# Kernel tuning notes

Hardware: AMD Instinct MI355X
Metric: run time of the kernel (lower is better)

The kernel has to match this reference:

```python
import jax, jax.numpy as jnp
import numpy as np

B, N_ATOMS, D_ATOM = 64, 256, 256
T_ANGLES = 2048
D_HID, D_OUT = 512, 256
BN_EPS = 1e-5


def setup_inputs() -> dict:
    key = jax.random.key(0)
    ks = jax.random.split(key, 8)
    z = jax.random.normal(ks[0], (B, N_ATOMS, D_ATOM), dtype=jnp.float32)
    # all entries valid (>=0) so the nonzero-selected row set is all B*T rows
    angel_atom_table = jax.random.randint(ks[1], (B, T_ANGLES, 3), 0, N_ATOMS, dtype=jnp.int64)
    W1 = jax.random.normal(ks[2], (D_ATOM, D_HID), dtype=jnp.float32) * (1.0 / np.sqrt(D_ATOM))
    b1 = jax.random.normal(ks[3], (D_HID,), dtype=jnp.float32) * 0.01
    gamma = jnp.ones((D_HID,), dtype=jnp.float32)
    beta = jnp.zeros((D_HID,), dtype=jnp.float32)
    W2 = jax.random.normal(ks[4], (D_HID, D_OUT), dtype=jnp.float32) * (1.0 / np.sqrt(D_HID))
    b2 = jax.random.normal(ks[5], (D_OUT,), dtype=jnp.float32) * 0.01
    return {"z": z, "angel_atom_table": angel_atom_table, "W1": W1, "b1": b1,
            "gamma": gamma, "beta": beta, "W2": W2, "b2": b2}


def reference(z, angel_atom_table, W1, b1, gamma, beta, W2, b2):
    Bb, Tt, _ = angel_atom_table.shape
    bi = jnp.arange(Bb)[:, None]                       # [B,1] broadcast batch index
    # gather 3 atom embeddings per angle and sum -> [B,T,d_atom]
    x = (z[bi, angel_atom_table[:, :, 0]]
         + z[bi, angel_atom_table[:, :, 1]]
         + z[bi, angel_atom_table[:, :, 2]])
    x = x.reshape(Bb * Tt, -1)                         # flattened valid rows (all valid)
    h = x @ W1 + b1                                    # Linear(d_atom, d_hid)
    mean = jnp.mean(h, axis=0)                         # BatchNorm1d (batch stats)
    var = jnp.var(h, axis=0)
    h = (h - mean) * jax.lax.rsqrt(var + BN_EPS) * gamma + beta
    h = jax.nn.relu(h)                                 # dropout inactive (eval)
    out = h @ W2 + b2                                  # Linear(d_hid, d_output)
    return out
```

## Files before the change

kernel.cpp:

```cpp
#include <hip/hip_runtime.h>

static constexpr int Bn  = 64;
static constexpr int T   = 2048;
static constexpr int NA  = 256;
static constexpr int DA  = 256;
static constexpr int DH  = 512;
static constexpr int DO  = 256;
static constexpr int M   = Bn * T;
static constexpr int NBS = M / 128;
static constexpr int NBC = M / 64;

typedef __attribute__((ext_vector_type(4))) float  f32x4;
typedef __attribute__((ext_vector_type(8))) __bf16 bf16x8;
typedef __attribute__((ext_vector_type(8))) short  short8;

__device__ __forceinline__ unsigned short f2bf(float f) {
  union { float f; unsigned u; } v; v.f = f;
  unsigned u = v.u + 0x7FFFu + ((v.u >> 16) & 1u);
  return (unsigned short)(u >> 16);
}
__device__ __forceinline__ float bf2f(unsigned short b) {
  union { unsigned u; float f; } v; v.u = ((unsigned)b) << 16;
  return v.f;
}

__device__ __forceinline__ void gl_lds16(const void* g, void* l) {
  __builtin_amdgcn_global_load_lds(
      (const __attribute__((address_space(1))) unsigned int*)g,
      (__attribute__((address_space(3))) unsigned int*)l, 16, 0, 0);
}

__global__ void prep_kernel(const float* __restrict__ W1, const float* __restrict__ W2,
                            unsigned short* __restrict__ W1T, unsigned short* __restrict__ W2T) {
  int id = blockIdx.x * 256 + threadIdx.x;
  {
    int n = id >> 8, k = id & 255;
    W1T[id] = f2bf(W1[k * DH + n]);
  }
  {
    int n = id >> 9, k = id & 511;
    W2T[id] = f2bf(W2[k * DO + n]);
  }
}

__global__ __launch_bounds__(256) void kA_zw(
    const float* __restrict__ z, const unsigned short* __restrict__ W1T,
    unsigned short* __restrict__ zW) {
  __shared__ __align__(16) unsigned short As[4][64][8];
  __shared__ __align__(16) unsigned short Bs[4][256][8];
  const int tid = threadIdx.x;
  const int bm = blockIdx.x >> 1, bn = blockIdx.x & 1;
  const int row0 = bm * 64, n0b = bn * 256;
  const int wave = tid >> 6, lane = tid & 63, ql = lane >> 4, r16 = lane & 15;
  const int am = tid >> 2, akq = tid & 3;
  const float* zrow = z + (size_t)(row0 + am) * DA + akq * 8;

  f32x4 acc[4][4] = {};

  for (int s = 0; s < 8; ++s) {
    const int k0 = s * 32;
#pragma unroll
    for (int i = 0; i < 4; ++i)
      gl_lds16(W1T + (size_t)(n0b + tid) * DA + k0 + i * 8,
               (unsigned short*)Bs + (size_t)(i * 256 + (tid & 192)) * 8);
    {
      float4 z0 = *(const float4*)(zrow + k0);
      float4 z1 = *(const float4*)(zrow + k0 + 4);
      short8 pk;
      pk[0] = (short)f2bf(z0.x); pk[1] = (short)f2bf(z0.y);
      pk[2] = (short)f2bf(z0.z); pk[3] = (short)f2bf(z0.w);
      pk[4] = (short)f2bf(z1.x); pk[5] = (short)f2bf(z1.y);
      pk[6] = (short)f2bf(z1.z); pk[7] = (short)f2bf(z1.w);
      *(short8*)&As[akq][am][0] = pk;
    }
    __syncthreads();
    bf16x8 afr[4], bfr[4];
#pragma unroll
    for (int mf = 0; mf < 4; ++mf) afr[mf] = *(const bf16x8*)&As[ql][mf * 16 + r16][0];
#pragma unroll
    for (int nf = 0; nf < 4; ++nf) bfr[nf] = *(const bf16x8*)&Bs[ql][wave * 64 + nf * 16 + r16][0];
#pragma unroll
    for (int mf = 0; mf < 4; ++mf)
#pragma unroll
      for (int nf = 0; nf < 4; ++nf)
        acc[mf][nf] = __builtin_amdgcn_mfma_f32_16x16x32_bf16(afr[mf], bfr[nf], acc[mf][nf], 0, 0, 0);
    __syncthreads();
  }

  const int n0 = n0b + wave * 64;
#pragma unroll
  for (int nf = 0; nf < 4; ++nf) {
    const int col = n0 + nf * 16 + r16;
#pragma unroll
    for (int mf = 0; mf < 4; ++mf)
#pragma unroll
      for (int p = 0; p < 4; ++p)
        zW[(size_t)(row0 + mf * 16 + ql * 4 + p) * DH + col] = f2bf(acc[mf][nf][p]);
  }
}

__global__ __launch_bounds__(256) void kB_stats(
    const unsigned short* __restrict__ zW, const int* __restrict__ tbl,
    float* __restrict__ psum, float* __restrict__ psq) {
  __shared__ int idxs[128][3];
  __shared__ float red1[4][512];
  __shared__ float red2[4][512];
  const int bid = blockIdx.x;
  const int blk = (bid & 7) * (NBS >> 3) + (bid >> 3);
  const int tid = threadIdx.x;
  const int row0 = blk * 128;
  const unsigned short* zWb = zW + (size_t)(row0 >> 11) * NA * DH;

  for (int i = tid; i < 384; i += 256) ((int*)idxs)[i] = tbl[(size_t)row0 * 3 + i];
  __syncthreads();

  const int cc = tid & 63, rg = tid >> 6;
  float s1[8] = {0, 0, 0, 0, 0, 0, 0, 0};
  float s2[8] = {0, 0, 0, 0, 0, 0, 0, 0};
#pragma unroll 4
  for (int i = 0; i < 32; ++i) {
    const int r = rg * 32 + i;
    const unsigned short* p0 = zWb + (size_t)idxs[r][0] * DH + cc * 8;
    const unsigned short* p1 = zWb + (size_t)idxs[r][1] * DH + cc * 8;
    const unsigned short* p2 = zWb + (size_t)idxs[r][2] * DH + cc * 8;
    short8 v0 = *(const short8*)p0;
    short8 v1 = *(const short8*)p1;
    short8 v2 = *(const short8*)p2;
#pragma unroll
    for (int j = 0; j < 8; ++j) {
      float h = bf2f((unsigned short)v0[j]) + bf2f((unsigned short)v1[j]) + bf2f((unsigned short)v2[j]);
      s1[j] += h;
      s2[j] = fmaf(h, h, s2[j]);
    }
  }
#pragma unroll
  for (int j = 0; j < 8; ++j) { red1[rg][cc * 8 + j] = s1[j]; red2[rg][cc * 8 + j] = s2[j]; }
  __syncthreads();
  for (int c = tid; c < 512; c += 256) {
    psum[(size_t)c * NBS + blk] = red1[0][c] + red1[1][c] + red1[2][c] + red1[3][c];
    psq [(size_t)c * NBS + blk] = red2[0][c] + red2[1][c] + red2[2][c] + red2[3][c];
  }
}

__global__ void k2_stats(const float* __restrict__ psum, const float* __restrict__ psq,
                         const float* __restrict__ gamma, const float* __restrict__ beta,
                         float* __restrict__ coef) {
  const int col = blockIdx.x, lane = threadIdx.x;
  float s1 = 0.f, s2 = 0.f;
  for (int i = lane; i < NBS; i += 64) {
    s1 += psum[(size_t)col * NBS + i];
    s2 += psq [(size_t)col * NBS + i];
  }
#pragma unroll
  for (int d = 1; d < 64; d <<= 1) { s1 += __shfl_xor(s1, d); s2 += __shfl_xor(s2, d); }
  if (lane == 0) {
    const float inv = 1.0f / (float)M;
    float mean = s1 * inv;
    float var  = s2 * inv - mean * mean;
    float a = gamma[col] * rsqrtf(var + 1e-5f);
    coef[col]      = a;
    coef[DH + col] = beta[col] - mean * a;
  }
}

__global__ __launch_bounds__(256) void kC_out(
    const unsigned short* __restrict__ zW, const int* __restrict__ tbl,
    const unsigned short* __restrict__ W2T, const float* __restrict__ coef,
    const float* __restrict__ b2, float* __restrict__ out) {
  __shared__ __align__(16) unsigned short As[4][64][8];
  __shared__ __align__(16) unsigned short Bs[4][256][8];
  __shared__ float aC[DH], dC[DH], bC[DO];
  __shared__ int idxs[64][3];

  const int bid = blockIdx.x;
  const int blk = (bid & 7) * (NBC >> 3) + (bid >> 3);
  const int tid = threadIdx.x;
  const int row0 = blk * 64;
  const unsigned short* zWb = zW + (size_t)(row0 >> 11) * NA * DH;

  if (tid < 192) ((int*)idxs)[tid] = tbl[(size_t)row0 * 3 + tid];
  aC[tid]       = coef[tid];            aC[tid + 256] = coef[tid + 256];
  dC[tid]       = coef[DH + tid];       dC[tid + 256] = coef[DH + tid + 256];
  bC[tid]       = b2[tid];
  __syncthreads();

  const int wave = tid >> 6, lane = tid & 63, ql = lane >> 4, r16 = lane & 15;
  const int am = tid >> 2, akq = tid & 3;

  const unsigned short* g0p = zWb + (size_t)idxs[am][0] * DH + akq * 8;
  const unsigned short* g1p = zWb + (size_t)idxs[am][1] * DH + akq * 8;
  const unsigned short* g2p = zWb + (size_t)idxs[am][2] * DH + akq * 8;
  short8 g0 = *(const short8*)g0p;
  short8 g1 = *(const short8*)g1p;
  short8 g2 = *(const short8*)g2p;

  f32x4 acc[4][4] = {};

  for (int s = 0; s < 16; ++s) {
    const int k0 = s * 32;
#pragma unroll
    for (int i = 0; i < 4; ++i)
      gl_lds16(W2T + (size_t)tid * DH + k0 + i * 8,
               (unsigned short*)Bs + (size_t)(i * 256 + (tid & 192)) * 8);
    {
      f32x4 av0 = *(const f32x4*)&aC[k0 + akq * 8];
      f32x4 av1 = *(const f32x4*)&aC[k0 + akq * 8 + 4];
      f32x4 dv0 = *(const f32x4*)&dC[k0 + akq * 8];
      f32x4 dv1 = *(const f32x4*)&dC[k0 + akq * 8 + 4];
      short8 pk;
#pragma unroll
      for (int j = 0; j < 8; ++j) {
        float h = bf2f((unsigned short)g0[j]) + bf2f((unsigned short)g1[j]) + bf2f((unsigned short)g2[j]);
        float a = (j < 4) ? av0[j] : av1[j - 4];
        float d = (j < 4) ? dv0[j] : dv1[j - 4];
        float f = fmaf(h, a, d);
        f = f > 0.f ? f : 0.f;
        pk[j] = (short)f2bf(f);
      }
      *(short8*)&As[akq][am][0] = pk;
    }
    __syncthreads();
    if (s < 15) {
      g0 = *(const short8*)(g0p + k0 + 32);
      g1 = *(const short8*)(g1p + k0 + 32);
      g2 = *(const short8*)(g2p + k0 + 32);
    }
    bf16x8 afr[4], bfr[4];
#pragma unroll
    for (int mf = 0; mf < 4; ++mf) afr[mf] = *(const bf16x8*)&As[ql][mf * 16 + r16][0];
#pragma unroll
    for (int nf = 0; nf < 4; ++nf) bfr[nf] = *(const bf16x8*)&Bs[ql][wave * 64 + nf * 16 + r16][0];
#pragma unroll
    for (int mf = 0; mf < 4; ++mf)
#pragma unroll
      for (int nf = 0; nf < 4; ++nf)
        acc[mf][nf] = __builtin_amdgcn_mfma_f32_16x16x32_bf16(afr[mf], bfr[nf], acc[mf][nf], 0, 0, 0);
    __syncthreads();
  }

  const int n0 = wave * 64;
#pragma unroll
  for (int nf = 0; nf < 4; ++nf) {
    const int col = n0 + nf * 16 + r16;
    const float bv = bC[col];
#pragma unroll
    for (int mf = 0; mf < 4; ++mf)
#pragma unroll
      for (int p = 0; p < 4; ++p)
        out[(size_t)(row0 + mf * 16 + ql * 4 + p) * DO + col] = acc[mf][nf][p] + bv;
  }
}

extern "C" void kernel_launch(void* const* d_in, const int* in_sizes, int n_in,
                              void* d_out, int out_size, void* d_ws, size_t ws_size,
                              hipStream_t stream) {
  const float* z     = (const float*)d_in[0];
  const int*   tbl   = (const int*)d_in[1];
  const float* W1    = (const float*)d_in[2];
  const float* gamma = (const float*)d_in[4];
  const float* beta  = (const float*)d_in[5];
  const float* W2    = (const float*)d_in[6];
  const float* b2    = (const float*)d_in[7];
  float* out = (float*)d_out;

  char* ws = (char*)d_ws;
  unsigned short* W1T  = (unsigned short*)(ws);
  unsigned short* W2T  = (unsigned short*)(ws + (256 << 10));
  float*          coef = (float*)(ws + (512 << 10));
  float*          psum = (float*)(ws + (1 << 20));
  float*          psq  = (float*)(ws + (3 << 20));
  unsigned short* zW   = (unsigned short*)(ws + (16 << 20));

  prep_kernel<<<512, 256, 0, stream>>>(W1, W2, W1T, W2T);
  kA_zw<<<512, 256, 0, stream>>>(z, W1T, zW);
  kB_stats<<<NBS, 256, 0, stream>>>(zW, tbl, psum, psq);
  k2_stats<<<DH, 64, 0, stream>>>(psum, psq, gamma, beta, coef);
  kC_out<<<NBC, 256, 0, stream>>>(zW, tbl, W2T, coef, b2, out);
}
```

Baseline: 282.8 us.

## Preload full A tile, double-buffer B with wave-local sync in GEMM kernels

New measurement: 272.1 us. -3.8%, faster.

```diff
diff --git a/kernel.cpp b/kernel.cpp
--- a/kernel.cpp
+++ b/kernel.cpp
@@ -46,45 +46,70 @@
 __global__ __launch_bounds__(256) void kA_zw(
     const float* __restrict__ z, const unsigned short* __restrict__ W1T,
     unsigned short* __restrict__ zW) {
-  __shared__ __align__(16) unsigned short As[4][64][8];
-  __shared__ __align__(16) unsigned short Bs[4][256][8];
+  __shared__ __align__(16) unsigned short As[32][64][8];
+  __shared__ __align__(16) unsigned short Bs[2][4][256][8];
   const int tid = threadIdx.x;
   const int bm = blockIdx.x >> 1, bn = blockIdx.x & 1;
   const int row0 = bm * 64, n0b = bn * 256;
   const int wave = tid >> 6, lane = tid & 63, ql = lane >> 4, r16 = lane & 15;
-  const int am = tid >> 2, akq = tid & 3;
-  const float* zrow = z + (size_t)(row0 + am) * DA + akq * 8;
-
-  f32x4 acc[4][4] = {};
-
-  for (int s = 0; s < 8; ++s) {
-    const int k0 = s * 32;
+  const int gr = tid >> 2, sub = tid & 3;
+  const int sxw = (sub << 2) ^ sub;
+  const int sxr = (ql << 2) ^ ql;
+
+  auto stageB = [&](int buf, int k0) {
 #pragma unroll
     for (int i = 0; i < 4; ++i)
       gl_lds16(W1T + (size_t)(n0b + tid) * DA + k0 + i * 8,
-               (unsigned short*)Bs + (size_t)(i * 256 + (tid & 192)) * 8);
-    {
-      float4 z0 = *(const float4*)(zrow + k0);
-      float4 z1 = *(const float4*)(zrow + k0 + 4);
-      short8 pk;
-      pk[0] = (short)f2bf(z0.x); pk[1] = (short)f2bf(z0.y);
-      pk[2] = (short)f2bf(z0.z); pk[3] = (short)f2bf(z0.w);
-      pk[4] = (short)f2bf(z1.x); pk[5] = (short)f2bf(z1.y);
-      pk[6] = (short)f2bf(z1.z); pk[7] = (short)f2bf(z1.w);
-      *(short8*)&As[akq][am][0] = pk;
-    }
-    __syncthreads();
+               (unsigned short*)Bs + (size_t)((buf * 4 + i) * 256 + wave * 64) * 8);
+  };
+
+  stageB(0, 0);
+
+  {
+    const float* zr = z + (size_t)(row0 + gr) * DA + sub * 8;
+    f32x4 za[16];
+#pragma unroll
+    for (int c = 0; c < 8; ++c) {
+      za[2 * c]     = *(const f32x4*)(zr + c * 32);
+      za[2 * c + 1] = *(const f32x4*)(zr + c * 32 + 4);
+    }
+#pragma unroll
+    for (int c = 0; c < 8; ++c) {
+      bf16x8 pk;
+#pragma unroll
+      for (int j = 0; j < 4; ++j) {
+        pk[j]     = (__bf16)za[2 * c][j];
+        pk[4 + j] = (__bf16)za[2 * c + 1][j];
+      }
+      *(bf16x8*)&As[c * 4 + sub][gr ^ sxw][0] = pk;
+    }
+  }
+  asm volatile("s_waitcnt lgkmcnt(0)" ::: "memory");
+  __builtin_amdgcn_s_barrier();
+
+  f32x4 acc[4][4] = {};
+  for (int s = 0; s < 8; ++s) {
+    asm volatile("s_waitcnt lgkmcnt(0)" ::: "memory");
+    if (s < 7) {
+      stageB((s + 1) & 1, (s + 1) * 32);
+      asm volatile("s_waitcnt vmcnt(4)" ::: "memory");
+    } else {
+      asm volatile("s_waitcnt vmcnt(0)" ::: "memory");
+    }
     bf16x8 afr[4], bfr[4];
 #pragma unroll
-    for (int mf = 0; mf < 4; ++mf) afr[mf] = *(const bf16x8*)&As[ql][mf * 16 + r16][0];
-#pragma unroll
-    for (int nf = 0; nf < 4; ++nf) bfr[nf] = *(const bf16x8*)&Bs[ql][wave * 64 + nf * 16 + r16][0];
+    for (int mf = 0; mf < 4; ++mf)
+      afr[mf] = *(const bf16x8*)&As[s * 4 + ql][(mf * 16 + r16) ^ sxr][0];
+#pragma unroll
+    for (int nf = 0; nf < 4; ++nf)
+      bfr[nf] = *(const bf16x8*)&Bs[s & 1][ql][wave * 64 + nf * 16 + r16][0];
+    __builtin_amdgcn_s_setprio(1);
 #pragma unroll
     for (int mf = 0; mf < 4; ++mf)
 #pragma unroll
       for (int nf = 0; nf < 4; ++nf)
         acc[mf][nf] = __builtin_amdgcn_mfma_f32_16x16x32_bf16(afr[mf], bfr[nf], acc[mf][nf], 0, 0, 0);
-    __syncthreads();
+    __builtin_amdgcn_s_setprio(0);
   }
 
   const int n0 = n0b + wave * 64;
@@ -117,7 +142,7 @@
   const int cc = tid & 63, rg = tid >> 6;
   float s1[8] = {0, 0, 0, 0, 0, 0, 0, 0};
   float s2[8] = {0, 0, 0, 0, 0, 0, 0, 0};
-#pragma unroll 4
+#pragma unroll 8
   for (int i = 0; i < 32; ++i) {
     const int r = rg * 32 + i;
     const unsigned short* p0 = zWb + (size_t)idxs[r][0] * DH + cc * 8;
@@ -167,8 +192,8 @@
     const unsigned short* __restrict__ zW, const int* __restrict__ tbl,
     const unsigned short* __restrict__ W2T, const float* __restrict__ coef,
     const float* __restrict__ b2, float* __restrict__ out) {
-  __shared__ __align__(16) unsigned short As[4][64][8];
-  __shared__ __align__(16) unsigned short Bs[4][256][8];
+  __shared__ __align__(16) unsigned short As[32][64][8];
+  __shared__ __align__(16) unsigned short Bs[2][4][256][8];
   __shared__ float aC[DH], dC[DH], bC[DO];
   __shared__ int idxs[64][3];
 
@@ -185,57 +210,86 @@
   __syncthreads();
 
   const int wave = tid >> 6, lane = tid & 63, ql = lane >> 4, r16 = lane & 15;
-  const int am = tid >> 2, akq = tid & 3;
-
-  const unsigned short* g0p = zWb + (size_t)idxs[am][0] * DH + akq * 8;
-  const unsigned short* g1p = zWb + (size_t)idxs[am][1] * DH + akq * 8;
-  const unsigned short* g2p = zWb + (size_t)idxs[am][2] * DH + akq * 8;
-  short8 g0 = *(const short8*)g0p;
-  short8 g1 = *(const short8*)g1p;
-  short8 g2 = *(const short8*)g2p;
-
-  f32x4 acc[4][4] = {};
-
-  for (int s = 0; s < 16; ++s) {
-    const int k0 = s * 32;
+  const int gr = tid >> 2, sub = tid & 3;
+  const int sxw = (sub << 2) ^ sub;
+  const int sxr = (ql << 2) ^ ql;
+
+  const unsigned short* g0p = zWb + (size_t)idxs[gr][0] * DH + sub * 8;
+  const unsigned short* g1p = zWb + (size_t)idxs[gr][1] * DH + sub * 8;
+  const unsigned short* g2p = zWb + (size_t)idxs[gr][2] * DH + sub * 8;
+
+  auto stageB = [&](int buf, int k0) {
 #pragma unroll
     for (int i = 0; i < 4; ++i)
       gl_lds16(W2T + (size_t)tid * DH + k0 + i * 8,
-               (unsigned short*)Bs + (size_t)(i * 256 + (tid & 192)) * 8);
-    {
-      f32x4 av0 = *(const f32x4*)&aC[k0 + akq * 8];
-      f32x4 av1 = *(const f32x4*)&aC[k0 + akq * 8 + 4];
-      f32x4 dv0 = *(const f32x4*)&dC[k0 + akq * 8];
-      f32x4 dv1 = *(const f32x4*)&dC[k0 + akq * 8 + 4];
-      short8 pk;
-#pragma unroll
-      for (int j = 0; j < 8; ++j) {
-        float h = bf2f((unsigned short)g0[j]) + bf2f((unsigned short)g1[j]) + bf2f((unsigned short)g2[j]);
-        float a = (j < 4) ? av0[j] : av1[j - 4];
-        float d = (j < 4) ? dv0[j] : dv1[j - 4];
-        float f = fmaf(h, a, d);
-        f = f > 0.f ? f : 0.f;
-        pk[j] = (short)f2bf(f);
+               (unsigned short*)Bs + (size_t)((buf * 4 + i) * 256 + wave * 64) * 8);
+  };
+
+  stageB(0, 0);
+
+  f32x4 acc[4][4] = {};
+
+  for (int h = 0; h < 2; ++h) {
+    const int kh = h * 256;
+    short8 v0[8], v1[8], v2[8];
+#pragma unroll
+    for (int c = 0; c < 8; ++c) {
+      v0[c] = *(const short8*)(g0p + kh + c * 32);
+      v1[c] = *(const short8*)(g1p + kh + c * 32);
+      v2[c] = *(const short8*)(g2p + kh + c * 32);
+    }
+    if (h) {
+      asm volatile("s_waitcnt lgkmcnt(0)" ::: "memory");
+      __builtin_amdgcn_s_barrier();
+    }
+#pragma unroll
+    for (int c = 0; c < 8; ++c) {
+      const int kk = kh + c * 32 + sub * 8;
+      f32x4 av0 = *(const f32x4*)&aC[kk];
+      f32x4 av1 = *(const f32x4*)&aC[kk + 4];
+      f32x4 dv0 = *(const f32x4*)&dC[kk];
+      f32x4 dv1 = *(const f32x4*)&dC[kk + 4];
+      bf16x8 pk;
+#pragma unroll
+      for (int j = 0; j < 4; ++j) {
+        float h0 = bf2f((unsigned short)v0[c][j]) + bf2f((unsigned short)v1[c][j]) + bf2f((unsigned short)v2[c][j]);
+        float f0 = fmaf(h0, av0[j], dv0[j]);
+        f0 = f0 > 0.f ? f0 : 0.f;
+        pk[j] = (__bf16)f0;
+        float h1 = bf2f((unsigned short)v0[c][4 + j]) + bf2f((unsigned short)v1[c][4 + j]) + bf2f((unsigned short)v2[c][4 + j]);
+        float f1 = fmaf(h1, av1[j], dv1[j]);
+        f1 = f1 > 0.f ? f1 : 0.f;
+        pk[4 + j] = (__bf16)f1;
       }
-      *(short8*)&As[akq][am][0] = pk;
-    }
-    __syncthreads();
-    if (s < 15) {
-      g0 = *(const short8*)(g0p + k0 + 32);
-      g1 = *(const short8*)(g1p + k0 + 32);
-      g2 = *(const short8*)(g2p + k0 + 32);
-    }
-    bf16x8 afr[4], bfr[4];
-#pragma unroll
-    for (int mf = 0; mf < 4; ++mf) afr[mf] = *(const bf16x8*)&As[ql][mf * 16 + r16][0];
-#pragma unroll
-    for (int nf = 0; nf < 4; ++nf) bfr[nf] = *(const bf16x8*)&Bs[ql][wave * 64 + nf * 16 + r16][0];
-#pragma unroll
-    for (int mf = 0; mf < 4; ++mf)
+      *(bf16x8*)&As[c * 4 + sub][gr ^ sxw][0] = pk;
+    }
+    asm volatile("s_waitcnt lgkmcnt(0)" ::: "memory");
+    __builtin_amdgcn_s_barrier();
+
+    for (int s = 0; s < 8; ++s) {
+      const int sg = h * 8 + s;
+      asm volatile("s_waitcnt lgkmcnt(0)" ::: "memory");
+      if (sg < 15) {
+        stageB((sg + 1) & 1, (sg + 1) * 32);
+        asm volatile("s_waitcnt vmcnt(4)" ::: "memory");
+      } else {
+        asm volatile("s_waitcnt vmcnt(0)" ::: "memory");
+      }
+      bf16x8 afr[4], bfr[4];
+#pragma unroll
+      for (int mf = 0; mf < 4; ++mf)
+        afr[mf] = *(const bf16x8*)&As[s * 4 + ql][(mf * 16 + r16) ^ sxr][0];
 #pragma unroll
       for (int nf = 0; nf < 4; ++nf)
-        acc[mf][nf] = __builtin_amdgcn_mfma_f32_16x16x32_bf16(afr[mf], bfr[nf], acc[mf][nf], 0, 0, 0);
-    __syncthreads();
+        bfr[nf] = *(const bf16x8*)&Bs[sg & 1][ql][wave * 64 + nf * 16 + r16][0];
+      __builtin_amdgcn_s_setprio(1);
+#pragma unroll
+      for (int mf = 0; mf < 4; ++mf)
+#pragma unroll
+        for (int nf = 0; nf < 4; ++nf)
+          acc[mf][nf] = __builtin_amdgcn_mfma_f32_16x16x32_bf16(afr[mf], bfr[nf], acc[mf][nf], 0, 0, 0);
+      __builtin_amdgcn_s_setprio(0);
+    }
   }
 
   const int n0 = wave * 64;
```
